# Optimization experiments

Measured on AMD Instinct MI355X. Metric: run time of the kernel, lower is better.

The kernel has to match this reference:

```python
import jax, jax.numpy as jnp
import numpy as np

N = 2_000_000  # number of 3x3 SPD matrices (DTI-scale volume)


def _make_spd(key, n):
    # M M^T + 0.5 I is symmetric positive definite with generically distinct eigenvalues
    m = jax.random.normal(key, (n, 3, 3), dtype=jnp.float32)
    return m @ jnp.swapaxes(m, -1, -2) + 0.5 * jnp.eye(3, dtype=jnp.float32)


def setup_inputs() -> dict:
    key = jax.random.key(0)
    k1, k2 = jax.random.split(key)
    return {"D1": _make_spd(k1, N), "D2": _make_spd(k2, N)}


def _logm_spd(D):
    # Batched symmetric matrix log via eigendecomposition: V diag(log w) V^T
    w, v = jnp.linalg.eigh(D)                    # w: [N,3], v: [N,3,3]
    return (v * jnp.log(w)[..., None, :]) @ jnp.swapaxes(v, -1, -2)


def reference(D1, D2):
    # Log-Euclidean SPD distance: ||logm(D1) - logm(D2)||_F, then mean of squares
    diff = _logm_spd(D1) - _logm_spd(D2)         # [N,3,3]
    sq_dist = jnp.sum(diff * diff, axis=(-1, -2))  # [N]
    return jnp.mean(sq_dist)
```

## Files before the change

kernel.cpp:

```cpp
#include <hip/hip_runtime.h>
#include <hip/hip_bf16.h>

#define BLOCK 256

__device__ __forceinline__ float frcp(float x) { return __builtin_amdgcn_rcpf(x); }
__device__ __forceinline__ float fsqrt(float x) { return __builtin_amdgcn_sqrtf(x); }

__device__ __forceinline__ float facos(float x) {
    float ax = fabsf(x);
    float sq = fsqrt(fmaxf(1.0f - ax, 0.0f));
    float poly = fmaf(fmaf(fmaf(-0.0187293f, ax, 0.0742610f), ax, -0.2121144f),
                      ax, 1.5707288f);
    float ac = sq * poly;
    return (x < 0.0f) ? (3.14159274f - ac) : ac;
}

__device__ __forceinline__ void logm3(const float m[6], float L[6]) {
    float a00 = m[0], a01 = m[1], a02 = m[2];
    float a11 = m[3], a12 = m[4], a22 = m[5];

    float q  = (a00 + a11 + a22) * (1.0f / 3.0f);
    float b00 = a00 - q, b11 = a11 - q, b22 = a22 - q;
    float p2 = b00*b00 + b11*b11 + b22*b22
             + 2.0f * (a01*a01 + a02*a02 + a12*a12);
    float p  = fsqrt(p2 * (1.0f / 6.0f));
    p = fmaxf(p, 1e-12f);
    float ip = frcp(p);
    float detB = b00*(b11*b22 - a12*a12)
               - a01*(a01*b22 - a12*a02)
               + a02*(a01*a12 - b11*a02);
    float ip3 = ip * ip * ip;
    float r = fminf(fmaxf(0.5f * detB * ip3, -1.0f), 1.0f);
    float phi = facos(r) * (1.0f / 3.0f);
    float sph = __sinf(phi), cph = __cosf(phi);
    float whi = q + 2.0f * p * cph;
    float wlo = q - p * (cph + 1.7320508f * sph);
    float wmid = 3.0f * q - whi - wlo;
    float w0 = fmaxf(wlo,  1e-8f);
    float w1 = fmaxf(wmid, 1e-8f);
    float w2 = fmaxf(whi,  1e-8f);

    float l0 = __logf(w0), l1 = __logf(w1), l2 = __logf(w2);
    float d01 = w1 - w0, d12 = w2 - w1, span = w2 - w0;
    float thr = 1e-3f * w1;
    float dd01 = (d01 > thr) ? (l1 - l0) * frcp(d01) : 2.0f * frcp(w0 + w1);
    float dd12 = (d12 > thr) ? (l2 - l1) * frcp(d12) : 2.0f * frcp(w1 + w2);
    float dd012 = (span > thr) ? (dd12 - dd01) * frcp(span)
                               : -0.5f * frcp(w1 * w1);
    float k2 = dd012;
    float k1 = dd01 - dd012 * (w0 + w1);
    float k0 = l0 - dd01 * w0 + dd012 * (w0 * w1);

    float s00 = a00*a00 + a01*a01 + a02*a02;
    float s01 = a00*a01 + a01*a11 + a02*a12;
    float s02 = a00*a02 + a01*a12 + a02*a22;
    float s11 = a01*a01 + a11*a11 + a12*a12;
    float s12 = a01*a02 + a11*a12 + a12*a22;
    float s22 = a02*a02 + a12*a12 + a22*a22;

    L[0] = k0 + k1*a00 + k2*s00;
    L[1] =      k1*a01 + k2*s01;
    L[2] =      k1*a02 + k2*s02;
    L[3] = k0 + k1*a11 + k2*s11;
    L[4] =      k1*a12 + k2*s12;
    L[5] = k0 + k1*a22 + k2*s22;
}

__device__ __forceinline__ void load6(const float* __restrict__ a, float m[6]) {
    m[0] = a[0]; m[1] = a[1]; m[2] = a[2];
    m[3] = a[4]; m[4] = a[5]; m[5] = a[8];
}

__device__ __forceinline__ float fnorm2_diff(const float L1[6], const float L2[6]) {
    float d0 = L1[0]-L2[0], d1 = L1[1]-L2[1], d2 = L1[2]-L2[2];
    float d3 = L1[3]-L2[3], d4 = L1[4]-L2[4], d5 = L1[5]-L2[5];
    return d0*d0 + d3*d3 + d5*d5 + 2.0f * (d1*d1 + d2*d2 + d4*d4);
}

__global__ void __launch_bounds__(BLOCK)
le_partial(const float* __restrict__ D1, const float* __restrict__ D2,
           float* __restrict__ partial, int n) {
    const int tid = threadIdx.x;
    const long stride = (long)gridDim.x * BLOCK;
    long i = (long)blockIdx.x * BLOCK + tid;
    float acc = 0.0f;

    float m1[6], m2[6];
    bool have = (i < n);
    if (have) { load6(D1 + i * 9, m1); load6(D2 + i * 9, m2); }

    while (have) {
        long inext = i + stride;
        bool hn = (inext < n);
        float n1[6], n2[6];
        if (hn) { load6(D1 + inext * 9, n1); load6(D2 + inext * 9, n2); }

        float L1[6], L2[6];
        logm3(m1, L1);
        logm3(m2, L2);
        acc += fnorm2_diff(L1, L2);

        #pragma unroll
        for (int k = 0; k < 6; ++k) { m1[k] = n1[k]; m2[k] = n2[k]; }
        i = inext;
        have = hn;
    }

    #pragma unroll
    for (int off = 32; off > 0; off >>= 1)
        acc += __shfl_down(acc, off, 64);
    __shared__ float wsum[BLOCK / 64];
    if ((tid & 63) == 0) wsum[tid >> 6] = acc;
    __syncthreads();
    if (tid == 0) {
        float s = 0.0f;
        #pragma unroll
        for (int i2 = 0; i2 < BLOCK / 64; ++i2) s += wsum[i2];
        partial[blockIdx.x] = s;
    }
}

__global__ void __launch_bounds__(BLOCK)
le_final(const float* __restrict__ partial, int nparts,
         float* __restrict__ out, double invN) {
    double s = 0.0;
    for (int i = threadIdx.x; i < nparts; i += BLOCK)
        s += (double)partial[i];
    #pragma unroll
    for (int off = 32; off > 0; off >>= 1)
        s += __shfl_down(s, off, 64);
    __shared__ double ws[BLOCK / 64];
    if ((threadIdx.x & 63) == 0) ws[threadIdx.x >> 6] = s;
    __syncthreads();
    if (threadIdx.x == 0) {
        double t = 0.0;
        #pragma unroll
        for (int i = 0; i < BLOCK / 64; ++i) t += ws[i];
        out[0] = (float)(t * invN);
    }
}

extern "C" void kernel_launch(void* const* d_in, const int* in_sizes, int n_in,
                              void* d_out, int out_size, void* d_ws, size_t ws_size,
                              hipStream_t stream) {
    const float* D1 = (const float*)d_in[0];
    const float* D2 = (const float*)d_in[1];
    float* out = (float*)d_out;
    float* partial = (float*)d_ws;

    int n = in_sizes[0] / 9;
    int nblk = (n + BLOCK - 1) / BLOCK;

    int grid = nblk < 2048 ? nblk : 2048;
    int maxblocks = (int)(ws_size / sizeof(float));
    if (maxblocks > 0 && grid > maxblocks) grid = maxblocks;
    if (grid < 1) grid = 1;

    le_partial<<<grid, BLOCK, 0, stream>>>(D1, D2, partial, n);
    le_final<<<1, BLOCK, 0, stream>>>(partial, grid, out, 1.0 / (double)n);
}
```

Before: 33.01 us.

## Unroll grid loop by two, use rsqrt, and branchless divided differences

The grid-stride loop now handles two matrix pairs per iteration with 32-bit indexing instead of software-prefetching one pair ahead, which exposes more independent work and more loads in flight. The eigenvalue scale now comes from a single rsqrt instead of sqrt plus reciprocal. The branchy divided-difference logic is replaced by clamped gaps that share one reciprocal, and the middle and top eigenvalue clamps are removed. This cuts transcendental and branch cost but may lose accuracy for nearly repeated eigenvalues, and int offsets rely on 9*n fitting in 32 bits.

```diff
diff --git a/kernel.cpp b/kernel.cpp
--- a/kernel.cpp
+++ b/kernel.cpp
@@ -2,9 +2,11 @@
 #include <hip/hip_bf16.h>
 
 #define BLOCK 256
+#define GRID  2048
 
 __device__ __forceinline__ float frcp(float x) { return __builtin_amdgcn_rcpf(x); }
 __device__ __forceinline__ float fsqrt(float x) { return __builtin_amdgcn_sqrtf(x); }
+__device__ __forceinline__ float frsq(float x) { return __builtin_amdgcn_rsqf(x); }
 
 __device__ __forceinline__ float facos(float x) {
     float ax = fabsf(x);
@@ -23,9 +25,9 @@
     float b00 = a00 - q, b11 = a11 - q, b22 = a22 - q;
     float p2 = b00*b00 + b11*b11 + b22*b22
              + 2.0f * (a01*a01 + a02*a02 + a12*a12);
-    float p  = fsqrt(p2 * (1.0f / 6.0f));
-    p = fmaxf(p, 1e-12f);
-    float ip = frcp(p);
+    float u  = fmaxf(p2 * (1.0f / 6.0f), 1e-24f);
+    float ip = frsq(u);
+    float p  = u * ip;
     float detB = b00*(b11*b22 - a12*a12)
                - a01*(a01*b22 - a12*a02)
                + a02*(a01*a12 - b11*a02);
@@ -36,17 +38,19 @@
     float whi = q + 2.0f * p * cph;
     float wlo = q - p * (cph + 1.7320508f * sph);
     float wmid = 3.0f * q - whi - wlo;
-    float w0 = fmaxf(wlo,  1e-8f);
-    float w1 = fmaxf(wmid, 1e-8f);
-    float w2 = fmaxf(whi,  1e-8f);
+    float w0 = fmaxf(wlo, 1e-6f);
+    float w1 = wmid;
+    float w2 = whi;
 
     float l0 = __logf(w0), l1 = __logf(w1), l2 = __logf(w2);
-    float d01 = w1 - w0, d12 = w2 - w1, span = w2 - w0;
-    float thr = 1e-3f * w1;
-    float dd01 = (d01 > thr) ? (l1 - l0) * frcp(d01) : 2.0f * frcp(w0 + w1);
-    float dd12 = (d12 > thr) ? (l2 - l1) * frcp(d12) : 2.0f * frcp(w1 + w2);
-    float dd012 = (span > thr) ? (dd12 - dd01) * frcp(span)
-                               : -0.5f * frcp(w1 * w1);
+    float e = 1e-4f * w2;
+    float d01 = fmaxf(w1 - w0, e);
+    float d12 = fmaxf(w2 - w1, e);
+    float d02 = fmaxf(w2 - w0, e);
+    float rP = frcp(d01 * d12 * d02);
+    float dd01 = (l1 - l0) * (d12 * d02) * rP;
+    float dd12 = (l2 - l1) * (d01 * d02) * rP;
+    float dd012 = (dd12 - dd01) * (d01 * d12) * rP;
     float k2 = dd012;
     float k1 = dd01 - dd012 * (w0 + w1);
     float k0 = l0 - dd01 * w0 + dd012 * (w0 * w1);
@@ -66,9 +70,11 @@
     L[5] = k0 + k1*a22 + k2*s22;
 }
 
-__device__ __forceinline__ void load6(const float* __restrict__ a, float m[6]) {
-    m[0] = a[0]; m[1] = a[1]; m[2] = a[2];
-    m[3] = a[4]; m[4] = a[5]; m[5] = a[8];
+__device__ __forceinline__ void load6i(const float* __restrict__ base, int off9,
+                                       float m[6]) {
+    __builtin_assume(off9 >= 0);
+    m[0] = base[off9 + 0]; m[1] = base[off9 + 1]; m[2] = base[off9 + 2];
+    m[3] = base[off9 + 4]; m[4] = base[off9 + 5]; m[5] = base[off9 + 8];
 }
 
 __device__ __forceinline__ float fnorm2_diff(const float L1[6], const float L2[6]) {
@@ -77,33 +83,35 @@
     return d0*d0 + d3*d3 + d5*d5 + 2.0f * (d1*d1 + d2*d2 + d4*d4);
 }
 
+__device__ __forceinline__ float pairdist(const float m1[6], const float m2[6]) {
+    float L1[6], L2[6];
+    logm3(m1, L1);
+    logm3(m2, L2);
+    return fnorm2_diff(L1, L2);
+}
+
 __global__ void __launch_bounds__(BLOCK)
 le_partial(const float* __restrict__ D1, const float* __restrict__ D2,
            float* __restrict__ partial, int n) {
     const int tid = threadIdx.x;
-    const long stride = (long)gridDim.x * BLOCK;
-    long i = (long)blockIdx.x * BLOCK + tid;
+    const int T = (int)gridDim.x * BLOCK;
     float acc = 0.0f;
 
-    float m1[6], m2[6];
-    bool have = (i < n);
-    if (have) { load6(D1 + i * 9, m1); load6(D2 + i * 9, m2); }
+    for (int base = (int)blockIdx.x * BLOCK + tid; base < n; base += 2 * T) {
+        int ia = base;
+        int ib = base + T;
+        bool hb = (ib < n);
+        int ibc = hb ? ib : ia;
 
-    while (have) {
-        long inext = i + stride;
-        bool hn = (inext < n);
-        float n1[6], n2[6];
-        if (hn) { load6(D1 + inext * 9, n1); load6(D2 + inext * 9, n2); }
+        float m1a[6], m2a[6], m1b[6], m2b[6];
+        load6i(D1, 9 * ia,  m1a);
+        load6i(D2, 9 * ia,  m2a);
+        load6i(D1, 9 * ibc, m1b);
+        load6i(D2, 9 * ibc, m2b);
 
-        float L1[6], L2[6];
-        logm3(m1, L1);
-        logm3(m2, L2);
-        acc += fnorm2_diff(L1, L2);
-
-        #pragma unroll
-        for (int k = 0; k < 6; ++k) { m1[k] = n1[k]; m2[k] = n2[k]; }
-        i = inext;
-        have = hn;
+        acc += pairdist(m1a, m2a);
+        float db = pairdist(m1b, m2b);
+        acc += hb ? db : 0.0f;
     }
 
     #pragma unroll
@@ -115,7 +123,7 @@
     if (tid == 0) {
         float s = 0.0f;
         #pragma unroll
-        for (int i2 = 0; i2 < BLOCK / 64; ++i2) s += wsum[i2];
+        for (int j = 0; j < BLOCK / 64; ++j) s += wsum[j];
         partial[blockIdx.x] = s;
     }
 }
@@ -149,9 +157,9 @@
     float* partial = (float*)d_ws;
 
     int n = in_sizes[0] / 9;
+    int grid = GRID;
     int nblk = (n + BLOCK - 1) / BLOCK;
-
-    int grid = nblk < 2048 ? nblk : 2048;
+    if (grid > nblk) grid = nblk;
     int maxblocks = (int)(ws_size / sizeof(float));
     if (maxblocks > 0 && grid > maxblocks) grid = maxblocks;
     if (grid < 1) grid = 1;
```

New measurement: 34.76 us. +5.3%, slower.
